# Optimization experiments

Measured on AMD Instinct MI355X. Metric: run time of the kernel, lower is better.

## Reference

```python
import jax, jax.numpy as jnp
import numpy as np

DIM = 512
HEADS = 8
HEAD_DIM = 64
INNER = HEADS * HEAD_DIM  # 512
FF = DIM * 2
EPS = 1e-5


def layernorm(x, g, b):
    mu = jnp.mean(x, axis=-1, keepdims=True)
    var = jnp.var(x, axis=-1, keepdims=True)
    return (x - mu) * jax.lax.rsqrt(var + EPS) * g + b


def setup_inputs() -> dict:
    key = jax.random.key(0)
    ks = jax.random.split(key, 10)
    s = lambda fan_in: 1.0 / np.sqrt(fan_in)
    return {
        "x": jax.random.normal(ks[0], (4, 2048, DIM), dtype=jnp.float32),
        "ln1_g": jnp.ones((DIM,), jnp.float32),
        "ln1_b": jnp.zeros((DIM,), jnp.float32),
        "w_qkv": jax.random.normal(ks[1], (DIM, 3 * INNER), jnp.float32) * s(DIM),
        "w_out": jax.random.normal(ks[2], (INNER, DIM), jnp.float32) * s(INNER),
        "b_out": jnp.zeros((DIM,), jnp.float32),
        "ln2_g": jnp.ones((DIM,), jnp.float32),
        "ln2_b": jnp.zeros((DIM,), jnp.float32),
        "w1": jax.random.normal(ks[3], (DIM, FF), jnp.float32) * s(DIM),
        "b1": jnp.zeros((FF,), jnp.float32),
        "w2": jax.random.normal(ks[4], (FF, DIM), jnp.float32) * s(FF),
        "b2": jnp.zeros((DIM,), jnp.float32),
    }


def reference(x, ln1_g, ln1_b, w_qkv, w_out, b_out, ln2_g, ln2_b, w1, b1, w2, b2):
    b, n, _ = x.shape
    # --- pre-LN MHSA ---
    h = layernorm(x, ln1_g, ln1_b)
    qkv = h @ w_qkv  # [b, n, 3*inner]
    q, k, v = jnp.split(qkv, 3, axis=-1)
    to_heads = lambda t: t.reshape(b, n, HEADS, HEAD_DIM).transpose(0, 2, 1, 3)
    q, k, v = to_heads(q), to_heads(k), to_heads(v)
    scores = jnp.einsum('bhid,bhjd->bhij', q, k) * (HEAD_DIM ** -0.5)
    attn = jax.nn.softmax(scores, axis=-1)
    attended = jnp.einsum('bhij,bhjd->bhid', attn, v)
    attended = attended.transpose(0, 2, 1, 3).reshape(b, n, INNER)
    x = attended @ w_out + b_out + x
    # --- pre-LN MLP ---
    h = layernorm(x, ln2_g, ln2_b)
    h = jax.nn.gelu(h @ w1 + b1, approximate=False)
    x = h @ w2 + b2 + x
    return x
```

## Files before the change

### kernel.cpp

```cpp
#include <hip/hip_runtime.h>
#include <math.h>


#define TOKENS 8192
#define SEQ    2048
typedef unsigned short u16;
typedef __attribute__((ext_vector_type(8))) _Float16 h8;
typedef __attribute__((ext_vector_type(4))) float f32x4;
typedef __attribute__((ext_vector_type(4))) unsigned short u16x4;

#define BAR_V0 asm volatile("s_waitcnt vmcnt(0) lgkmcnt(0)\n\ts_barrier" ::: "memory")

__device__ __forceinline__ u16 f2h(float f) {
    _Float16 h = (_Float16)f;
    return __builtin_bit_cast(u16, h);
}
__device__ __forceinline__ void a16(void* lds, const void* g) {
    __builtin_amdgcn_global_load_lds(
        (const __attribute__((address_space(1))) unsigned int*)g,
        (__attribute__((address_space(3))) unsigned int*)lds, 16, 0, 0);
}
__device__ __forceinline__ float gelu_exact(float v) {
    return 0.5f * v * (1.0f + erff(v * 0.70710678118654752f));
}

__global__ __launch_bounds__(256) void prep_k(const float* __restrict__ wqkv,
                                              const float* __restrict__ wout,
                                              const float* __restrict__ w1,
                                              const float* __restrict__ w2,
                                              u16* __restrict__ dqkv,
                                              u16* __restrict__ dout,
                                              u16* __restrict__ d1,
                                              u16* __restrict__ d2,
                                              const float* __restrict__ x,
                                              const float* __restrict__ g,
                                              const float* __restrict__ bta,
                                              u16* __restrict__ oh) {
    const int tid = threadIdx.x;
    if (blockIdx.x >= 512) {
        const int lane = tid & 63;
        const int row  = ((blockIdx.x - 512) << 2) + (tid >> 6);
        const float* xr = x + ((size_t)row << 9) + (lane << 3);
        float v[8];
        *(float4*)&v[0] = *(const float4*)xr;
        *(float4*)&v[4] = *(const float4*)(xr + 4);
        float s = 0.f, ss = 0.f;
#pragma unroll
        for (int i = 0; i < 8; i++) { s += v[i]; ss += v[i] * v[i]; }
#pragma unroll
        for (int m = 32; m; m >>= 1) {
            s  += __shfl_xor(s, m, 64);
            ss += __shfl_xor(ss, m, 64);
        }
        const float mu   = s * (1.0f / 512.0f);
        const float rstd = rsqrtf(ss * (1.0f / 512.0f) - mu * mu + 1e-5f);
        float gg[8], bb[8];
        *(float4*)&gg[0] = *(const float4*)(g + (lane << 3));
        *(float4*)&gg[4] = *(const float4*)(g + (lane << 3) + 4);
        *(float4*)&bb[0] = *(const float4*)(bta + (lane << 3));
        *(float4*)&bb[4] = *(const float4*)(bta + (lane << 3) + 4);
        union { u16 us[8]; uint4 q; } H;
#pragma unroll
        for (int i = 0; i < 8; i++) H.us[i] = f2h((v[i] - mu) * rstd * gg[i] + bb[i]);
        *(uint4*)&oh[((size_t)row << 9) + (lane << 3)] = H.q;
        return;
    }
    __shared__ float t[64][65];
    int b = blockIdx.x;
    const float* src; u16* dst; int K, N, n0, k0;
    if (b < 192)      { src = wqkv; dst = dqkv; K = 512;  N = 1536; n0 = (b % 24) << 6; k0 = (b / 24) << 6; }
    else if (b < 256) { b -= 192; src = wout; dst = dout; K = 512;  N = 512;  n0 = (b & 7) << 6;  k0 = (b >> 3) << 6; }
    else if (b < 384) { b -= 256; src = w1;   dst = d1;   K = 512;  N = 1024; n0 = (b & 15) << 6; k0 = (b >> 4) << 6; }
    else              { b -= 384; src = w2;   dst = d2;   K = 1024; N = 512;  n0 = (b & 7) << 6;  k0 = (b >> 3) << 6; }
    {
        const int kr = tid >> 2, nc = (tid & 3) << 4;
        const float* p = src + (size_t)(k0 + kr) * N + n0 + nc;
#pragma unroll
        for (int i = 0; i < 4; i++)
            *(float4*)&t[kr][nc + (i << 2)] = *(const float4*)(p + (i << 2));
    }
    __syncthreads();
    {
        const int nr = tid >> 2, kc = (tid & 3) << 4;
        union { u16 us[16]; uint4 q[2]; } H;
#pragma unroll
        for (int i = 0; i < 16; i++) H.us[i] = f2h(t[kc + i][nr]);
        const size_t o = (size_t)(n0 + nr) * K + k0 + kc;
        *(uint4*)&dst[o] = H.q[0];
        *(uint4*)&dst[o + 8] = H.q[1];
    }
}

__global__ __launch_bounds__(256) void ln_k(const float* __restrict__ x,
                                            const float* __restrict__ g,
                                            const float* __restrict__ bta,
                                            u16* __restrict__ oh) {
    const int lane = threadIdx.x & 63;
    const int row  = (blockIdx.x << 2) + (threadIdx.x >> 6);
    const float* xr = x + ((size_t)row << 9) + (lane << 3);
    float v[8];
    *(float4*)&v[0] = *(const float4*)xr;
    *(float4*)&v[4] = *(const float4*)(xr + 4);
    float s = 0.f, ss = 0.f;
#pragma unroll
    for (int i = 0; i < 8; i++) { s += v[i]; ss += v[i] * v[i]; }
#pragma unroll
    for (int m = 32; m; m >>= 1) {
        s  += __shfl_xor(s, m, 64);
        ss += __shfl_xor(ss, m, 64);
    }
    const float mu   = s * (1.0f / 512.0f);
    const float rstd = rsqrtf(ss * (1.0f / 512.0f) - mu * mu + 1e-5f);
    float gg[8], bb[8];
    *(float4*)&gg[0] = *(const float4*)(g + (lane << 3));
    *(float4*)&gg[4] = *(const float4*)(g + (lane << 3) + 4);
    *(float4*)&bb[0] = *(const float4*)(bta + (lane << 3));
    *(float4*)&bb[4] = *(const float4*)(bta + (lane << 3) + 4);
    union { u16 us[8]; uint4 q; } H;
#pragma unroll
    for (int i = 0; i < 8; i++) H.us[i] = f2h((v[i] - mu) * rstd * gg[i] + bb[i]);
    *(uint4*)&oh[((size_t)row << 9) + (lane << 3)] = H.q;
}

template <int EPI>
__global__ __launch_bounds__(256, 3) void sgemm_k(
    const u16* __restrict__ A, const u16* __restrict__ B,
    const float* __restrict__ bias, const float* __restrict__ res,
    float* __restrict__ Cf, u16* __restrict__ Ch, u16* __restrict__ Dh,
    int M, int N, int K) {
    __shared__ u16 sm[16384];
    const int tid = threadIdx.x;
    const int lane = tid & 63, wv = tid >> 6;
    const int col = lane & 15, quad = lane >> 4;
    const int wm = (wv & 1) << 6, wn = (wv >> 1) << 6;
    const int bm = blockIdx.y << 7, bn = blockIdx.x << 7;

    const int r0 = tid >> 2,         c0 = (tid & 3) ^ ((r0 >> 1) & 3);
    const int r1 = (tid + 256) >> 2, c1 = (tid & 3) ^ ((r1 >> 1) & 3);
    const u16* Ag0 = A + (size_t)(bm + r0) * K + c0 * 8;
    const u16* Ag1 = A + (size_t)(bm + r1) * K + c1 * 8;
    const u16* Bg0 = B + (size_t)(bn + r0) * K + c0 * 8;
    const u16* Bg1 = B + (size_t)(bn + r1) * K + c1 * 8;
    const int lw0 = wv * 512, lw1 = wv * 512 + 2048;
    const int swz = (col >> 1) & 3;
    const f32x4 z4 = {0.f, 0.f, 0.f, 0.f};
    f32x4 acc[4][4] = {{z4,z4,z4,z4},{z4,z4,z4,z4},{z4,z4,z4,z4},{z4,z4,z4,z4}};

    a16(&sm[lw0],        Ag0);  a16(&sm[lw1],        Ag1);
    a16(&sm[lw0 + 4096], Bg0);  a16(&sm[lw1 + 4096], Bg1);

    int ib = 0;
    for (int k0 = 0; k0 < K; k0 += 32, ib ^= 1) {
        BAR_V0;
        if (k0 + 32 < K) {
            const int nb = (ib ^ 1) * 8192;
            const int kn = k0 + 32;
            a16(&sm[nb + lw0],        Ag0 + kn);  a16(&sm[nb + lw1],        Ag1 + kn);
            a16(&sm[nb + lw0 + 4096], Bg0 + kn);  a16(&sm[nb + lw1 + 4096], Bg1 + kn);
        }
        const int cb = ib * 8192;
        h8 af[4];
#pragma unroll
        for (int mt = 0; mt < 4; mt++) {
            const int ra = cb + (wm + (mt << 4) + col) * 32 + ((quad ^ swz) << 3);
            af[mt] = *(const h8*)&sm[ra];
        }
#pragma unroll
        for (int nt = 0; nt < 4; nt++) {
            const int rb = cb + 4096 + (wn + (nt << 4) + col) * 32 + ((quad ^ swz) << 3);
            h8 bf = *(const h8*)&sm[rb];
#pragma unroll
            for (int mt = 0; mt < 4; mt++)
                acc[mt][nt] = __builtin_amdgcn_mfma_f32_16x16x32_f16(af[mt], bf, acc[mt][nt], 0, 0, 0);
        }
    }

    if constexpr (EPI == 0) {
        if (bn >= 1024) {
            const int hd0  = (bn - 1024) >> 6;
            const int b8   = (bm >> 11) << 3;
            const int keyb = bm & 2047;
            __syncthreads();
#pragma unroll
            for (int hf = 0; hf < 2; hf++) {
                if ((wv >> 1) == hf) {
#pragma unroll
                    for (int mt = 0; mt < 4; mt++)
#pragma unroll
                    for (int rr = 0; rr < 4; rr++) {
                        const int key = wm + (mt << 4) + (quad << 2) + rr;
#pragma unroll
                        for (int nt = 0; nt < 4; nt++) {
                            const int dl = (nt << 4) + col;
                            sm[dl * 136 + key] = f2h(acc[mt][nt][rr]);
                        }
                    }
                }
                __syncthreads();
                {
                    const int d = tid >> 2;
#pragma unroll
                    for (int c = 0; c < 4; c++) {
                        const int key0 = ((((tid & 3) << 2) + c) << 3);
                        const size_t gb = ((size_t)(b8 + hd0 + hf) << 17)
                                        + ((size_t)d << 11) + keyb + key0;
                        *(uint4*)&Dh[gb] = *(const uint4*)&sm[d * 136 + key0];
                    }
                }
                __syncthreads();
            }
            return;
        }
    }

    float bs[4];
    if constexpr (EPI >= 1) {
#pragma unroll
        for (int nt = 0; nt < 4; nt++) bs[nt] = bias[bn + wn + (nt << 4) + col];
    }
#pragma unroll
    for (int mt = 0; mt < 4; mt++) {
#pragma unroll
        for (int rr = 0; rr < 4; rr++) {
            const int row = bm + wm + (mt << 4) + (quad << 2) + rr;
#pragma unroll
            for (int nt = 0; nt < 4; nt++) {
                const int colg = bn + wn + (nt << 4) + col;
                float v = acc[mt][nt][rr];
                if constexpr (EPI == 0) {
                    const int b = row >> 11, key = row & 2047;
                    if (bn < 512) {
                        Cf[((size_t)row << 9) + colg] = v;
                    } else {
                        const int hd = (colg - 512) >> 6, d = colg & 63;
                        Ch[((size_t)((b << 3) + hd) << 17) + (key << 6) + d] = f2h(v);
                    }
                } else if constexpr (EPI == 2) {
                    Ch[(size_t)row * N + colg] = f2h(gelu_exact(v + bs[nt]));
                } else {
                    const size_t o = (size_t)row * N + colg;
                    Cf[o] = v + bs[nt] + res[o];
                }
            }
        }
    }
}

__global__ __launch_bounds__(128, 2) void attn_k(const float* __restrict__ q,
                                                 const u16* __restrict__ kh,
                                                 const u16* __restrict__ vth,
                                                 u16* __restrict__ ah) {
    __shared__ u16 sm[20480];
    const int tid = threadIdx.x;
    const int lane = tid & 63, wv = tid >> 6;
    const int col = lane & 15, quad = lane >> 4;
    const int qt = blockIdx.x, bh = blockIdx.y;
    const int b = bh >> 3, h = bh & 7;
    const size_t tok0 = (size_t)b * SEQ;
    const size_t bhK = (size_t)bh << 17;
    const int q0 = qt << 6;

    h8 qf[2][2];
#pragma unroll
    for (int sub = 0; sub < 2; sub++) {
        const int qrow = q0 + (wv << 5) + (sub << 4) + col;
        const float* qp = q + ((tok0 + qrow) << 9) + (h << 6) + (quad << 3);
#pragma unroll
        for (int kc = 0; kc < 2; kc++) {
            float v[8];
            *(float4*)&v[0] = *(const float4*)(qp + (kc << 5));
            *(float4*)&v[4] = *(const float4*)(qp + (kc << 5) + 4);
            union { u16 us[8]; h8 v8; } H;
#pragma unroll
            for (int i = 0; i < 8; i++) H.us[i] = f2h(v[i] * 0.125f);
            qf[sub][kc] = H.v8;
        }
    }

    const f32x4 z4 = {0.f, 0.f, 0.f, 0.f};
    f32x4 o[2][4] = {{z4, z4, z4, z4}, {z4, z4, z4, z4}};
    float m_run[2] = {-1e30f, -1e30f}, l_run[2] = {0.f, 0.f};

    size_t kbz[4], vbz[4];
    int doff[4];
#pragma unroll
    for (int j = 0; j < 4; j++) {
        const int C = (((j << 1) + wv) << 6) + lane;
        const int sr = C >> 3, sp = (C & 7) ^ (sr & 7);
        kbz[j] = bhK + ((size_t)sr << 6) + (sp << 3);
        vbz[j] = bhK + ((size_t)sr << 11) + (sp << 3);
        doff[j] = (((j << 1) + wv) << 9);
    }

#pragma unroll
    for (int j = 0; j < 4; j++) a16(&sm[doff[j]], kh + kbz[j]);
#pragma unroll
    for (int j = 0; j < 4; j++) a16(&sm[8192 + doff[j]], vth + vbz[j]);
#pragma unroll
    for (int j = 0; j < 4; j++) a16(&sm[4096 + doff[j]], kh + kbz[j] + 4096);

    int ib = 0;
    for (int jt = 0; jt < 32; jt++, ib ^= 1) {
        if (jt < 31) {
            asm volatile("s_waitcnt vmcnt(4) lgkmcnt(0)\n\ts_barrier" ::: "memory");
        } else {
            asm volatile("s_waitcnt vmcnt(0) lgkmcnt(0)\n\ts_barrier" ::: "memory");
        }
        if (jt < 31) {
            const size_t vo = (size_t)(jt + 1) << 6;
            const int vb = 8192 + ((ib ^ 1) << 12);
#pragma unroll
            for (int j = 0; j < 4; j++) a16(&sm[vb + doff[j]], vth + vbz[j] + vo);
        }

        const int cb = ib << 12;
        f32x4 st0[4] = {z4, z4, z4, z4}, st1[4] = {z4, z4, z4, z4};
        __builtin_amdgcn_s_setprio(1);
#pragma unroll
        for (int kb = 0; kb < 4; kb++) {
            const int key = (kb << 4) + col;
            const int r64 = key << 6, k7 = key & 7;
#pragma unroll
            for (int kc = 0; kc < 2; kc++) {
                const int ofs = cb + r64 + ((((kc << 2) + quad) ^ k7) << 3);
                h8 kf = *(const h8*)&sm[ofs];
                st0[kb] = __builtin_amdgcn_mfma_f32_16x16x32_f16(kf, qf[0][kc], st0[kb], 0, 0, 0);
                st1[kb] = __builtin_amdgcn_mfma_f32_16x16x32_f16(kf, qf[1][kc], st1[kb], 0, 0, 0);
            }
        }
        __builtin_amdgcn_s_setprio(0);

#pragma unroll
        for (int sub = 0; sub < 2; sub++) {
            f32x4* st = sub ? st1 : st0;
            float mx = st[0][0];
#pragma unroll
            for (int kb = 0; kb < 4; kb++)
#pragma unroll
                for (int r = 0; r < 4; r++) mx = fmaxf(mx, st[kb][r]);
            mx = fmaxf(mx, __shfl_xor(mx, 16));
            mx = fmaxf(mx, __shfl_xor(mx, 32));
            const float mn = fmaxf(m_run[sub], mx);
            const float alp = __expf(m_run[sub] - mn);
            m_run[sub] = mn;
            float p[16];
            float rs = 0.0f;
#pragma unroll
            for (int kb = 0; kb < 4; kb++)
#pragma unroll
                for (int r = 0; r < 4; r++) {
                    float e = __expf(st[kb][r] - mn);
                    p[(kb << 2) + r] = e;
                    rs += e;
                }
            rs += __shfl_xor(rs, 16);
            rs += __shfl_xor(rs, 32);
            l_run[sub] = l_run[sub] * alp + rs;
            float aO[4];
#pragma unroll
            for (int r = 0; r < 4; r++) aO[r] = __shfl(alp, (quad << 2) + r);
#pragma unroll
            for (int db = 0; db < 4; db++) {
                o[sub][db][0] *= aO[0]; o[sub][db][1] *= aO[1];
                o[sub][db][2] *= aO[2]; o[sub][db][3] *= aO[3];
            }
            const int prow = (wv << 5) + (sub << 4) + col;
            const int p64 = prow << 6, p7 = prow & 7;
#pragma unroll
            for (int kb = 0; kb < 4; kb++) {
                u16x4 hv;
#pragma unroll
                for (int r = 0; r < 4; r++) hv[r] = f2h(p[(kb << 2) + r]);
                const int c = (kb << 1) + (quad >> 1);
                *(u16x4*)&sm[16384 + p64 + ((c ^ p7) << 3) + ((quad & 1) << 2)] = hv;
            }
        }

        asm volatile("s_waitcnt lgkmcnt(0)\n\ts_barrier" ::: "memory");

        if (jt < 30) {
            const size_t ko = (size_t)(jt + 2) << 12;
            const int kb2 = ib << 12;
#pragma unroll
            for (int j = 0; j < 4; j++) a16(&sm[kb2 + doff[j]], kh + kbz[j] + ko);
        }

        h8 pf[2][2];
#pragma unroll
        for (int sub = 0; sub < 2; sub++) {
            const int prow = (wv << 5) + (sub << 4) + col;
            const int p64 = prow << 6, p7 = prow & 7;
#pragma unroll
            for (int kc = 0; kc < 2; kc++)
                pf[sub][kc] = *(const h8*)&sm[16384 + p64 + ((((kc << 2) + quad) ^ p7) << 3)];
        }
        const int vbase = 8192 + (ib << 12);
        __builtin_amdgcn_s_setprio(1);
#pragma unroll
        for (int db = 0; db < 4; db++) {
            const int d = (db << 4) + col;
            const int v64 = vbase + (d << 6), d7 = d & 7;
#pragma unroll
            for (int kc = 0; kc < 2; kc++) {
                h8 vf = *(const h8*)&sm[v64 + ((((kc << 2) + quad) ^ d7) << 3)];
                o[0][db] = __builtin_amdgcn_mfma_f32_16x16x32_f16(pf[0][kc], vf, o[0][db], 0, 0, 0);
                o[1][db] = __builtin_amdgcn_mfma_f32_16x16x32_f16(pf[1][kc], vf, o[1][db], 0, 0, 0);
            }
        }
        __builtin_amdgcn_s_setprio(0);
    }

#pragma unroll
    for (int sub = 0; sub < 2; sub++) {
        float linv[4];
#pragma unroll
        for (int r = 0; r < 4; r++) linv[r] = 1.0f / __shfl(l_run[sub], (quad << 2) + r);
#pragma unroll
        for (int r = 0; r < 4; r++) {
            const size_t rowo = ((tok0 + q0 + (wv << 5) + (sub << 4) + (quad << 2) + r) << 9)
                                + (h << 6) + col;
#pragma unroll
            for (int db = 0; db < 4; db++)
                ah[rowo + (db << 4)] = f2h(o[sub][db][r] * linv[r]);
        }
    }
}

extern "C" void kernel_launch(void* const* d_in, const int* in_sizes, int n_in,
                              void* d_out, int out_size, void* d_ws, size_t ws_size,
                              hipStream_t stream) {
    const float* x     = (const float*)d_in[0];
    const float* ln1_g = (const float*)d_in[1];
    const float* ln1_b = (const float*)d_in[2];
    const float* w_qkv = (const float*)d_in[3];
    const float* w_out = (const float*)d_in[4];
    const float* b_out = (const float*)d_in[5];
    const float* ln2_g = (const float*)d_in[6];
    const float* ln2_b = (const float*)d_in[7];
    const float* w1    = (const float*)d_in[8];
    const float* b1    = (const float*)d_in[9];
    const float* w2    = (const float*)d_in[10];
    const float* b2    = (const float*)d_in[11];
    float* out = (float*)d_out;

    u16* wqkvh = (u16*)d_ws;
    u16* wouth = wqkvh + 1536 * 512;
    u16* w1h   = wouth + 512 * 512;
    u16* w2h   = w1h + 1024 * 512;
    u16* hbuf  = w2h + 512 * 1024;
    float* qbuf = (float*)(hbuf + (size_t)TOKENS * 512);
    float* x2   = qbuf;
    u16* kh  = (u16*)(qbuf + (size_t)TOKENS * 512);
    u16* vth = kh + (size_t)32 * 131072;
    u16* gh  = kh;

    prep_k<<<2560, 256, 0, stream>>>(w_qkv, w_out, w1, w2, wqkvh, wouth, w1h, w2h,
                                     x, ln1_g, ln1_b, hbuf);
    sgemm_k<0><<<dim3(12, 64), 256, 0, stream>>>(hbuf, wqkvh, nullptr, nullptr,
                                                 qbuf, kh, vth, TOKENS, 1536, 512);
    attn_k<<<dim3(32, 32), 128, 0, stream>>>(qbuf, kh, vth, hbuf);
    sgemm_k<1><<<dim3(4, 64), 256, 0, stream>>>(hbuf, wouth, b_out, x,
                                                x2, nullptr, nullptr, TOKENS, 512, 512);
    ln_k<<<TOKENS / 4, 256, 0, stream>>>(x2, ln2_g, ln2_b, hbuf);
    sgemm_k<2><<<dim3(8, 64), 256, 0, stream>>>(hbuf, w1h, b1, nullptr,
                                                nullptr, gh, nullptr, TOKENS, 1024, 512);
    sgemm_k<3><<<dim3(4, 64), 256, 0, stream>>>(gh, w2h, b2, x2,
                                                out, nullptr, nullptr, TOKENS, 512, 1024);
}
```

Before: 248.4 us.

## Split attention query tile across four waves of 16 rows each

The attention kernel now launches 256 threads (4 waves) per block instead of 128, with each wave owning 16 query rows rather than 32. Per-wave registers for scores, outputs and softmax state are halved, and K/V tile loads are spread over more threads. The aim is higher occupancy and latency hiding, at the cost of less reuse of each K/V fragment per wave, since each LDS read now feeds one MFMA instead of two.

```diff
diff --git a/kernel.cpp b/kernel.cpp
--- a/kernel.cpp
+++ b/kernel.cpp
@@ -246,7 +246,7 @@
     }
 }
 
-__global__ __launch_bounds__(128, 2) void attn_k(const float* __restrict__ q,
+__global__ __launch_bounds__(256, 4) void attn_k(const float* __restrict__ q,
                                                  const u16* __restrict__ kh,
                                                  const u16* __restrict__ vth,
                                                  u16* __restrict__ ah) {
@@ -260,10 +260,9 @@
     const size_t bhK = (size_t)bh << 17;
     const int q0 = qt << 6;
 
-    h8 qf[2][2];
-#pragma unroll
-    for (int sub = 0; sub < 2; sub++) {
-        const int qrow = q0 + (wv << 5) + (sub << 4) + col;
+    h8 qf[2];
+    {
+        const int qrow = q0 + (wv << 4) + col;
         const float* qp = q + ((tok0 + qrow) << 9) + (h << 6) + (quad << 3);
 #pragma unroll
         for (int kc = 0; kc < 2; kc++) {
@@ -273,36 +272,36 @@
             union { u16 us[8]; h8 v8; } H;
 #pragma unroll
             for (int i = 0; i < 8; i++) H.us[i] = f2h(v[i] * 0.125f);
-            qf[sub][kc] = H.v8;
+            qf[kc] = H.v8;
         }
     }
 
     const f32x4 z4 = {0.f, 0.f, 0.f, 0.f};
-    f32x4 o[2][4] = {{z4, z4, z4, z4}, {z4, z4, z4, z4}};
-    float m_run[2] = {-1e30f, -1e30f}, l_run[2] = {0.f, 0.f};
-
-    size_t kbz[4], vbz[4];
-    int doff[4];
-#pragma unroll
-    for (int j = 0; j < 4; j++) {
-        const int C = (((j << 1) + wv) << 6) + lane;
+    f32x4 o[4] = {z4, z4, z4, z4};
+    float m_run = -1e30f, l_run = 0.f;
+
+    size_t kbz[2], vbz[2];
+    int doff[2];
+#pragma unroll
+    for (int j = 0; j < 2; j++) {
+        const int C = (((j << 2) + wv) << 6) + lane;
         const int sr = C >> 3, sp = (C & 7) ^ (sr & 7);
         kbz[j] = bhK + ((size_t)sr << 6) + (sp << 3);
         vbz[j] = bhK + ((size_t)sr << 11) + (sp << 3);
-        doff[j] = (((j << 1) + wv) << 9);
-    }
-
-#pragma unroll
-    for (int j = 0; j < 4; j++) a16(&sm[doff[j]], kh + kbz[j]);
-#pragma unroll
-    for (int j = 0; j < 4; j++) a16(&sm[8192 + doff[j]], vth + vbz[j]);
-#pragma unroll
-    for (int j = 0; j < 4; j++) a16(&sm[4096 + doff[j]], kh + kbz[j] + 4096);
+        doff[j] = (((j << 2) + wv) << 9);
+    }
+
+#pragma unroll
+    for (int j = 0; j < 2; j++) a16(&sm[doff[j]], kh + kbz[j]);
+#pragma unroll
+    for (int j = 0; j < 2; j++) a16(&sm[8192 + doff[j]], vth + vbz[j]);
+#pragma unroll
+    for (int j = 0; j < 2; j++) a16(&sm[4096 + doff[j]], kh + kbz[j] + 4096);
 
     int ib = 0;
     for (int jt = 0; jt < 32; jt++, ib ^= 1) {
         if (jt < 31) {
-            asm volatile("s_waitcnt vmcnt(4) lgkmcnt(0)\n\ts_barrier" ::: "memory");
+            asm volatile("s_waitcnt vmcnt(2) lgkmcnt(0)\n\ts_barrier" ::: "memory");
         } else {
             asm volatile("s_waitcnt vmcnt(0) lgkmcnt(0)\n\ts_barrier" ::: "memory");
         }
@@ -310,11 +309,11 @@
             const size_t vo = (size_t)(jt + 1) << 6;
             const int vb = 8192 + ((ib ^ 1) << 12);
 #pragma unroll
-            for (int j = 0; j < 4; j++) a16(&sm[vb + doff[j]], vth + vbz[j] + vo);
+            for (int j = 0; j < 2; j++) a16(&sm[vb + doff[j]], vth + vbz[j] + vo);
         }
 
         const int cb = ib << 12;
-        f32x4 st0[4] = {z4, z4, z4, z4}, st1[4] = {z4, z4, z4, z4};
+        f32x4 st[4] = {z4, z4, z4, z4};
         __builtin_amdgcn_s_setprio(1);
 #pragma unroll
         for (int kb = 0; kb < 4; kb++) {
@@ -324,56 +323,51 @@
             for (int kc = 0; kc < 2; kc++) {
                 const int ofs = cb + r64 + ((((kc << 2) + quad) ^ k7) << 3);
                 h8 kf = *(const h8*)&sm[ofs];
-                st0[kb] = __builtin_amdgcn_mfma_f32_16x16x32_f16(kf, qf[0][kc], st0[kb], 0, 0, 0);
-                st1[kb] = __builtin_amdgcn_mfma_f32_16x16x32_f16(kf, qf[1][kc], st1[kb], 0, 0, 0);
+                st[kb] = __builtin_amdgcn_mfma_f32_16x16x32_f16(kf, qf[kc], st[kb], 0, 0, 0);
             }
         }
         __builtin_amdgcn_s_setprio(0);
 
-#pragma unroll
-        for (int sub = 0; sub < 2; sub++) {
-            f32x4* st = sub ? st1 : st0;
-            float mx = st[0][0];
-#pragma unroll
-            for (int kb = 0; kb < 4; kb++)
-#pragma unroll
-                for (int r = 0; r < 4; r++) mx = fmaxf(mx, st[kb][r]);
-            mx = fmaxf(mx, __shfl_xor(mx, 16));
-            mx = fmaxf(mx, __shfl_xor(mx, 32));
-            const float mn = fmaxf(m_run[sub], mx);
-            const float alp = __expf(m_run[sub] - mn);
-            m_run[sub] = mn;
-            float p[16];
-            float rs = 0.0f;
-#pragma unroll
-            for (int kb = 0; kb < 4; kb++)
-#pragma unroll
-                for (int r = 0; r < 4; r++) {
-                    float e = __expf(st[kb][r] - mn);
-                    p[(kb << 2) + r] = e;
-                    rs += e;
-                }
-            rs += __shfl_xor(rs, 16);
-            rs += __shfl_xor(rs, 32);
-            l_run[sub] = l_run[sub] * alp + rs;
-            float aO[4];
-#pragma unroll
-            for (int r = 0; r < 4; r++) aO[r] = __shfl(alp, (quad << 2) + r);
-#pragma unroll
-            for (int db = 0; db < 4; db++) {
-                o[sub][db][0] *= aO[0]; o[sub][db][1] *= aO[1];
-                o[sub][db][2] *= aO[2]; o[sub][db][3] *= aO[3];
+        float mx = st[0][0];
+#pragma unroll
+        for (int kb = 0; kb < 4; kb++)
+#pragma unroll
+            for (int r = 0; r < 4; r++) mx = fmaxf(mx, st[kb][r]);
+        mx = fmaxf(mx, __shfl_xor(mx, 16));
+        mx = fmaxf(mx, __shfl_xor(mx, 32));
+        const float mn = fmaxf(m_run, mx);
+        const float alp = __expf(m_run - mn);
+        m_run = mn;
+        float p[16];
+        float rs = 0.0f;
+#pragma unroll
+        for (int kb = 0; kb < 4; kb++)
+#pragma unroll
+            for (int r = 0; r < 4; r++) {
+                float e = __expf(st[kb][r] - mn);
+                p[(kb << 2) + r] = e;
+                rs += e;
             }
-            const int prow = (wv << 5) + (sub << 4) + col;
-            const int p64 = prow << 6, p7 = prow & 7;
-#pragma unroll
-            for (int kb = 0; kb < 4; kb++) {
-                u16x4 hv;
-#pragma unroll
-                for (int r = 0; r < 4; r++) hv[r] = f2h(p[(kb << 2) + r]);
-                const int c = (kb << 1) + (quad >> 1);
-                *(u16x4*)&sm[16384 + p64 + ((c ^ p7) << 3) + ((quad & 1) << 2)] = hv;
-            }
+        rs += __shfl_xor(rs, 16);
+        rs += __shfl_xor(rs, 32);
+        l_run = l_run * alp + rs;
+        float aO[4];
+#pragma unroll
+        for (int r = 0; r < 4; r++) aO[r] = __shfl(alp, (quad << 2) + r);
+#pragma unroll
+        for (int db = 0; db < 4; db++) {
+            o[db][0] *= aO[0]; o[db][1] *= aO[1];
+            o[db][2] *= aO[2]; o[db][3] *= aO[3];
+        }
+        const int prow = (wv << 4) + col;
+        const int p64 = prow << 6, p7 = prow & 7;
+#pragma unroll
+        for (int kb = 0; kb < 4; kb++) {
+            u16x4 hv;
+#pragma unroll
+            for (int r = 0; r < 4; r++) hv[r] = f2h(p[(kb << 2) + r]);
+            const int c = (kb << 1) + (quad >> 1);
+            *(u16x4*)&sm[16384 + p64 + ((c ^ p7) << 3) + ((quad & 1) << 2)] = hv;
         }
 
         asm volatile("s_waitcnt lgkmcnt(0)\n\ts_barrier" ::: "memory");
@@ -382,18 +376,14 @@
             const size_t ko = (size_t)(jt + 2) << 12;
             const int kb2 = ib << 12;
 #pragma unroll
-            for (int j = 0; j < 4; j++) a16(&sm[kb2 + doff[j]], kh + kbz[j] + ko);
-        }
-
-        h8 pf[2][2];
-#pragma unroll
-        for (int sub = 0; sub < 2; sub++) {
-            const int prow = (wv << 5) + (sub << 4) + col;
-            const int p64 = prow << 6, p7 = prow & 7;
-#pragma unroll
-            for (int kc = 0; kc < 2; kc++)
-                pf[sub][kc] = *(const h8*)&sm[16384 + p64 + ((((kc << 2) + quad) ^ p7) << 3)];
-        }
+            for (int j = 0; j < 2; j++) a16(&sm[kb2 + doff[j]], kh + kbz[j] + ko);
+        }
+
+        h8 pf[2];
+#pragma unroll
+        for (int kc = 0; kc < 2; kc++)
+            pf[kc] = *(const h8*)&sm[16384 + p64 + ((((kc << 2) + quad) ^ p7) << 3)];
+
         const int vbase = 8192 + (ib << 12);
         __builtin_amdgcn_s_setprio(1);
 #pragma unroll
@@ -403,26 +393,22 @@
 #pragma unroll
             for (int kc = 0; kc < 2; kc++) {
                 h8 vf = *(const h8*)&sm[v64 + ((((kc << 2) + quad) ^ d7) << 3)];
-                o[0][db] = __builtin_amdgcn_mfma_f32_16x16x32_f16(pf[0][kc], vf, o[0][db], 0, 0, 0);
-                o[1][db] = __builtin_amdgcn_mfma_f32_16x16x32_f16(pf[1][kc], vf, o[1][db], 0, 0, 0);
+                o[db] = __builtin_amdgcn_mfma_f32_16x16x32_f16(pf[kc], vf, o[db], 0, 0, 0);
             }
         }
         __builtin_amdgcn_s_setprio(0);
     }
 
-#pragma unroll
-    for (int sub = 0; sub < 2; sub++) {
-        float linv[4];
-#pragma unroll
-        for (int r = 0; r < 4; r++) linv[r] = 1.0f / __shfl(l_run[sub], (quad << 2) + r);
-#pragma unroll
-        for (int r = 0; r < 4; r++) {
-            const size_t rowo = ((tok0 + q0 + (wv << 5) + (sub << 4) + (quad << 2) + r) << 9)
-                                + (h << 6) + col;
-#pragma unroll
-            for (int db = 0; db < 4; db++)
-                ah[rowo + (db << 4)] = f2h(o[sub][db][r] * linv[r]);
-        }
+    float linv[4];
+#pragma unroll
+    for (int r = 0; r < 4; r++) linv[r] = 1.0f / __shfl(l_run, (quad << 2) + r);
+#pragma unroll
+    for (int r = 0; r < 4; r++) {
+        const size_t rowo = ((tok0 + q0 + (wv << 4) + (quad << 2) + r) << 9)
+                            + (h << 6) + col;
+#pragma unroll
+        for (int db = 0; db < 4; db++)
+            ah[rowo + (db << 4)] = f2h(o[db][r] * linv[r]);
     }
 }
 
@@ -458,7 +444,7 @@
                                      x, ln1_g, ln1_b, hbuf);
     sgemm_k<0><<<dim3(12, 64), 256, 0, stream>>>(hbuf, wqkvh, nullptr, nullptr,
                                                  qbuf, kh, vth, TOKENS, 1536, 512);
-    attn_k<<<dim3(32, 32), 128, 0, stream>>>(qbuf, kh, vth, hbuf);
+    attn_k<<<dim3(32, 32), 256, 0, stream>>>(qbuf, kh, vth, hbuf);
     sgemm_k<1><<<dim3(4, 64), 256, 0, stream>>>(hbuf, wouth, b_out, x,
                                                 x2, nullptr, nullptr, TOKENS, 512, 512);
     ln_k<<<TOKENS / 4, 256, 0, stream>>>(x2, ln2_g, ln2_b, hbuf);
```

After: 249.4 us. No clear change (+0.4%).
